# Kernel optimization log

Hardware: AMD Instinct MI355X
Metric: run time of the kernel (lower is better)

The kernel has to match this reference:

```python
import jax, jax.numpy as jnp
import numpy as np

B, N, IN_DIM = 32, 8192, 128
H, C = 4, 32
NEG_SLOPE = 0.2


def _xavier(key, shape, fan_in, fan_out):
    limit = np.sqrt(6.0 / (fan_in + fan_out))
    return jax.random.uniform(key, shape, minval=-limit, maxval=limit, dtype=jnp.float32)


def setup_inputs() -> dict:
    key = jax.random.key(0)
    k_x, k_wl, k_wr, k_att = jax.random.split(key, 4)
    x = jax.random.normal(k_x, (B, N, IN_DIM), dtype=jnp.float32)
    W_l = _xavier(k_wl, (IN_DIM, H * C), IN_DIM, H * C)
    b_l = jnp.zeros((H * C,), dtype=jnp.float32)
    W_r = _xavier(k_wr, (IN_DIM, H * C), IN_DIM, H * C)
    b_r = jnp.zeros((H * C,), dtype=jnp.float32)
    att = _xavier(k_att, (H, C), H, C)
    return {"x": x, "W_l": W_l, "b_l": b_l, "W_r": W_r, "b_r": b_r, "att": att}


def reference(x, W_l, b_l, W_r, b_r, att):
    Bs, Ns, _ = x.shape
    # Dense projections -> [B, N, H, C]
    x_l = (x @ W_l + b_l).reshape(Bs, Ns, H, C)
    x_r = (x @ W_r + b_r).reshape(Bs, Ns, H, C)
    # GATv2 additive score for edges (j -> center 0): LeakyReLU(x_l[0] + x_r[j])
    e = jax.nn.leaky_relu(x_l[:, :1, :, :] + x_r, negative_slope=NEG_SLOPE)  # [B,N,H,C]
    logits = jnp.einsum('bnhc,hc->bnh', e, att)  # [B,N,H]
    alpha = jax.nn.softmax(logits, axis=1)
    # Weighted aggregation into the center node; others keep their self-loop x_r
    m_center = jnp.sum(alpha[..., None] * x_r, axis=1, keepdims=True)  # [B,1,H,C]
    out = x_r.at[:, :1, :, :].set(m_center)
    return out.reshape(Bs, Ns, H * C)
```

## Files before the change

kernel.cpp:

```cpp
#include <hip/hip_runtime.h>

#define BATCH 32
#define NROWS 8192
#define IND   128
#define HC    128
#define NEG   0.2f
#define NBLK  32
#define ROWS  64
#define ITERS (NROWS / (NBLK * ROWS))
#define PART_STRIDE 136

typedef __attribute__((ext_vector_type(8))) short short8;
typedef __attribute__((ext_vector_type(4))) float f32x4;

#define BARRIER() asm volatile("s_waitcnt lgkmcnt(0)\n\ts_barrier" ::: "memory")

__device__ __forceinline__ unsigned short f2bf(float f) {
    unsigned u = __float_as_uint(f);
    u += 0x7FFFu + ((u >> 16) & 1u);
    return (unsigned short)(u >> 16);
}
__device__ __forceinline__ unsigned pack2(float a, float b) {
    return (unsigned)f2bf(a) | ((unsigned)f2bf(b) << 16);
}

__global__ void gat_center(const float* __restrict__ x, const float* __restrict__ Wl,
                           const float* __restrict__ bl, float* __restrict__ xl0)
{
    const int b = blockIdx.x, t = threadIdx.x;
    __shared__ float xrow[128];
    xrow[t] = x[(size_t)b * NROWS * IND + t];
    __syncthreads();
    float acc = bl[t];
#pragma unroll 16
    for (int k = 0; k < 128; ++k) acc = fmaf(xrow[k], Wl[k * 128 + t], acc);
    xl0[b * 128 + t] = acc;
}

__global__ __launch_bounds__(256, 3) void gat_main(
    const float* __restrict__ x, const float* __restrict__ Wr,
    const float* __restrict__ br, const float* __restrict__ att,
    const float* __restrict__ xl0, float* __restrict__ out,
    float* __restrict__ part)
{
    const int tid  = threadIdx.x;
    const int lane = tid & 63;
    const int wv   = tid >> 6;
    const int b    = blockIdx.x >> 5;
    const int blk  = blockIdx.x & (NBLK - 1);

    __shared__ float ubuf[64 * 132];
    __shared__ float w_s[64][4];
    __shared__ float wmax_s[4][4];
    __shared__ float wsum_s[4][4];
    __shared__ float Mrun_s[4], Srun_s[4], scale_s[4];
    __shared__ float Prun_s[128];
    __shared__ float ptmp_s[2][128];
    __shared__ float xl0_s[128], att_s[128], br_s[128];

    unsigned short* Asw = (unsigned short*)ubuf;
    float (*xr_s)[132]  = (float(*)[132])ubuf;

    const int pr[4] = { (tid) >> 4, (tid + 256) >> 4, (tid + 512) >> 4, (tid + 768) >> 4 };
    const int pk    = (tid & 15) << 3;

    float4 pf[4][2];
    {
        const float* xr0 = x + ((size_t)b * NROWS + blk * (ITERS * ROWS)) * IND;
#pragma unroll
        for (int ii = 0; ii < 4; ++ii) {
            pf[ii][0] = *(const float4*)(xr0 + pr[ii] * IND + pk);
            pf[ii][1] = *(const float4*)(xr0 + pr[ii] * IND + pk + 4);
        }
    }

    for (int i = tid; i < 128 * 128; i += 256) {
        int n = i & 127, k = i >> 7;
        Asw[n * 128 + (k ^ ((n & 7) << 3))] = f2bf(Wr[k * 128 + n]);
    }
    if (tid < 128) {
        xl0_s[tid]  = xl0[b * 128 + tid];
        att_s[tid]  = att[tid];
        br_s[tid]   = br[tid];
        Prun_s[tid] = 0.f;
    }
    if (tid < 4) { Mrun_s[tid] = -INFINITY; Srun_s[tid] = 0.f; }
    BARRIER();

    short8 bfr[2][4];
    {
        const int ksel = lane >> 4;
#pragma unroll
        for (int ct = 0; ct < 2; ++ct) {
            const int n  = wv * 32 + ct * 16 + (lane & 15);
            const int sw = (n & 7) << 3;
#pragma unroll
            for (int ks = 0; ks < 4; ++ks) {
                int k0 = ks * 32 + ksel * 8;
                bfr[ct][ks] = *(const short8*)&Asw[n * 128 + (k0 ^ sw)];
            }
        }
    }
    BARRIER();

    const int lr = tid >> 2, lh = tid & 3;

    for (int it = 0; it < ITERS; ++it) {
        const int n0 = blk * (ITERS * ROWS) + it * ROWS;

#pragma unroll
        for (int ii = 0; ii < 4; ++ii) {
            uint4 u;
            u.x = pack2(pf[ii][0].x, pf[ii][0].y); u.y = pack2(pf[ii][0].z, pf[ii][0].w);
            u.z = pack2(pf[ii][1].x, pf[ii][1].y); u.w = pack2(pf[ii][1].z, pf[ii][1].w);
            *(uint4*)&Asw[pr[ii] * 128 + (pk ^ ((pr[ii] & 7) << 3))] = u;
        }
        BARRIER();

        f32x4 acc[4][2];
#pragma unroll
        for (int i = 0; i < 4; ++i)
#pragma unroll
            for (int j = 0; j < 2; ++j) acc[i][j] = (f32x4){0.f, 0.f, 0.f, 0.f};
        {
            const int ksel = lane >> 4;
#pragma unroll
            for (int rt = 0; rt < 4; ++rt) {
                const int rA  = rt * 16 + (lane & 15);
                const int swa = (rA & 7) << 3;
                short8 afr[4];
#pragma unroll
                for (int ks = 0; ks < 4; ++ks) {
                    int k0 = ks * 32 + ksel * 8;
                    afr[ks] = *(const short8*)&Asw[rA * 128 + (k0 ^ swa)];
                }
#pragma unroll
                for (int ct = 0; ct < 2; ++ct)
#pragma unroll
                    for (int ks = 0; ks < 4; ++ks)
                        acc[rt][ct] = __builtin_amdgcn_mfma_f32_16x16x32_bf16(
                            afr[ks], bfr[ct][ks], acc[rt][ct], 0, 0, 0);
            }
        }
        BARRIER();

        {
            const int rq = (lane >> 4) * 4;
            const int cb = lane & 15;
#pragma unroll
            for (int rt = 0; rt < 4; ++rt)
#pragma unroll
                for (int ct = 0; ct < 2; ++ct) {
                    const int col  = wv * 32 + ct * 16 + cb;
                    const float bias = br_s[col];
#pragma unroll
                    for (int rg = 0; rg < 4; ++rg)
                        xr_s[rt * 16 + rq + rg][col] = acc[rt][ct][rg] + bias;
                }
        }
        BARRIER();

        if (it + 1 < ITERS) {
            const float* xr0 = x + ((size_t)b * NROWS + n0 + ROWS) * IND;
#pragma unroll
            for (int ii = 0; ii < 4; ++ii) {
                pf[ii][0] = *(const float4*)(xr0 + pr[ii] * IND + pk);
                pf[ii][1] = *(const float4*)(xr0 + pr[ii] * IND + pk + 4);
            }
        }

        {
            float* ob = out + ((size_t)b * NROWS + n0) * HC;
#pragma unroll
            for (int j = 0; j < 8; ++j) {
                int idx = tid + j * 256;
                int row = idx >> 5, c4 = (idx & 31) << 2;
                *(float4*)(ob + row * HC + c4) = *(const float4*)&xr_s[row][c4];
            }
        }

        float lg = 0.f;
        {
            const float* xp = &xr_s[lr][lh * 32];
            const float* ap = &att_s[lh * 32];
            const float* qp = &xl0_s[lh * 32];
#pragma unroll
            for (int c4 = 0; c4 < 32; c4 += 4) {
                float4 xv = *(const float4*)(xp + c4);
                float4 av = *(const float4*)(ap + c4);
                float4 qv = *(const float4*)(qp + c4);
                float v0 = qv.x + xv.x; v0 = v0 > 0.f ? v0 : NEG * v0;
                float v1 = qv.y + xv.y; v1 = v1 > 0.f ? v1 : NEG * v1;
                float v2 = qv.z + xv.z; v2 = v2 > 0.f ? v2 : NEG * v2;
                float v3 = qv.w + xv.w; v3 = v3 > 0.f ? v3 : NEG * v3;
                lg = fmaf(v0, av.x, fmaf(v1, av.y, fmaf(v2, av.z, fmaf(v3, av.w, lg))));
            }
        }

        float mx = lg;
#pragma unroll
        for (int mk = 4; mk < 64; mk <<= 1) mx = fmaxf(mx, __shfl_xor(mx, mk));
        if (lane < 4) wmax_s[wv][lane] = mx;
        BARRIER();

        const float Mblk = fmaxf(fmaxf(wmax_s[0][lh], wmax_s[1][lh]),
                                 fmaxf(wmax_s[2][lh], wmax_s[3][lh]));
        const float Mold = Mrun_s[lh];
        const float Mnew = fmaxf(Mold, Mblk);
        const float w    = __expf(lg - Mnew);
        w_s[lr][lh] = w;
        float swv = w;
#pragma unroll
        for (int mk = 4; mk < 64; mk <<= 1) swv += __shfl_xor(swv, mk);
        if (lane < 4) wsum_s[wv][lane] = swv;
        BARRIER();

        if (tid < 4) {
            const float sc = __expf(Mold - Mnew);
            scale_s[tid] = sc;
            Srun_s[tid]  = Srun_s[tid] * sc +
                (wsum_s[0][tid] + wsum_s[1][tid] + wsum_s[2][tid] + wsum_s[3][tid]);
            Mrun_s[tid]  = Mnew;
        }
        {
            const int hc = tid & 127, half = tid >> 7;
            const int h2 = hc >> 5;
            float accp = 0.f;
#pragma unroll 8
            for (int i2 = 0; i2 < 32; ++i2) {
                int rr = half * 32 + i2;
                accp = fmaf(w_s[rr][h2], xr_s[rr][hc], accp);
            }
            ptmp_s[half][hc] = accp;
        }
        BARRIER();
        if (tid < 128)
            Prun_s[tid] = Prun_s[tid] * scale_s[tid >> 5] + ptmp_s[0][tid] + ptmp_s[1][tid];
    }

    float* pb = part + (size_t)(b * NBLK + blk) * PART_STRIDE;
    if (tid < 4)   { pb[tid] = Mrun_s[tid]; pb[4 + tid] = Srun_s[tid]; }
    if (tid < 128) pb[8 + tid] = Prun_s[tid];
}

__global__ void gat_final(const float* __restrict__ part, float* __restrict__ out)
{
    const int b = blockIdx.x, t = threadIdx.x;
    const int h = t >> 5;
    const float* pb = part + (size_t)b * NBLK * PART_STRIDE;
    float Mg = -INFINITY;
    for (int i = 0; i < NBLK; ++i) Mg = fmaxf(Mg, pb[i * PART_STRIDE + h]);
    float Sg = 0.f, Pg = 0.f;
    for (int i = 0; i < NBLK; ++i) {
        const float sc = __expf(pb[i * PART_STRIDE + h] - Mg);
        Sg += pb[i * PART_STRIDE + 4 + h] * sc;
        Pg  = fmaf(pb[i * PART_STRIDE + 8 + t], sc, Pg);
    }
    out[(size_t)b * NROWS * HC + t] = Pg / Sg;
}

extern "C" void kernel_launch(void* const* d_in, const int* in_sizes, int n_in,
                              void* d_out, int out_size, void* d_ws, size_t ws_size,
                              hipStream_t stream)
{
    const float* x   = (const float*)d_in[0];
    const float* Wl  = (const float*)d_in[1];
    const float* bl  = (const float*)d_in[2];
    const float* Wr  = (const float*)d_in[3];
    const float* br  = (const float*)d_in[4];
    const float* att = (const float*)d_in[5];
    float* out = (float*)d_out;

    float* xl0  = (float*)d_ws;
    float* part = xl0 + BATCH * 128;

    gat_center<<<BATCH, 128, 0, stream>>>(x, Wl, bl, xl0);
    gat_main<<<BATCH * NBLK, 256, 0, stream>>>(x, Wr, br, att, xl0, out, part);
    gat_final<<<BATCH, 128, 0, stream>>>(part, out);
}
```

Measured before the change: 79.96 us.

## Split gat_main into more, smaller blocks and load W_r fragments directly from global

Raises the blocks per batch from 32 to 128, with 32-row tiles and 2 iterations, and raises the occupancy hint to 6 blocks per CU. Each block now builds its bf16 W_r MFMA fragments straight from global memory rather than transposing the whole matrix through LDS. Softmax running state moves from shared memory into registers, and several per-iteration barriers are removed. The aim is better latency hiding and cheaper per-block setup, at the cost of more partial records for the final reduction kernel to combine and redundant W_r reads across more blocks.

```diff
diff --git a/kernel.cpp b/kernel.cpp
--- a/kernel.cpp
+++ b/kernel.cpp
@@ -5,9 +5,9 @@
 #define IND   128
 #define HC    128
 #define NEG   0.2f
-#define NBLK  32
-#define ROWS  64
-#define ITERS (NROWS / (NBLK * ROWS))
+#define NBLK  128
+#define ROWS  32
+#define ITERS 2
 #define PART_STRIDE 136
 
 typedef __attribute__((ext_vector_type(8))) short short8;
@@ -37,7 +37,7 @@
     xl0[b * 128 + t] = acc;
 }
 
-__global__ __launch_bounds__(256, 3) void gat_main(
+__global__ __launch_bounds__(256, 6) void gat_main(
     const float* __restrict__ x, const float* __restrict__ Wr,
     const float* __restrict__ br, const float* __restrict__ att,
     const float* __restrict__ xl0, float* __restrict__ out,
@@ -46,86 +46,80 @@
     const int tid  = threadIdx.x;
     const int lane = tid & 63;
     const int wv   = tid >> 6;
-    const int b    = blockIdx.x >> 5;
+    const int b    = blockIdx.x >> 7;
     const int blk  = blockIdx.x & (NBLK - 1);
 
-    __shared__ float ubuf[64 * 132];
-    __shared__ float w_s[64][4];
-    __shared__ float wmax_s[4][4];
-    __shared__ float wsum_s[4][4];
-    __shared__ float Mrun_s[4], Srun_s[4], scale_s[4];
-    __shared__ float Prun_s[128];
+    __shared__ float ubuf[ROWS * 132];
+    __shared__ float wmax_s[2][4], wsum_s[2][4];
     __shared__ float ptmp_s[2][128];
-    __shared__ float xl0_s[128], att_s[128], br_s[128];
+    __shared__ float xl0_s[128], att_s[128];
 
     unsigned short* Asw = (unsigned short*)ubuf;
     float (*xr_s)[132]  = (float(*)[132])ubuf;
 
-    const int pr[4] = { (tid) >> 4, (tid + 256) >> 4, (tid + 512) >> 4, (tid + 768) >> 4 };
-    const int pk    = (tid & 15) << 3;
-
-    float4 pf[4][2];
+    const int pr0 = tid >> 4, pr1 = (tid + 256) >> 4;
+    const int pk  = (tid & 15) << 3;
+    const size_t xorg = ((size_t)b * NROWS + (size_t)blk * (ITERS * ROWS)) * IND;
+
+    float4 pf[2][2];
     {
-        const float* xr0 = x + ((size_t)b * NROWS + blk * (ITERS * ROWS)) * IND;
-#pragma unroll
-        for (int ii = 0; ii < 4; ++ii) {
-            pf[ii][0] = *(const float4*)(xr0 + pr[ii] * IND + pk);
-            pf[ii][1] = *(const float4*)(xr0 + pr[ii] * IND + pk + 4);
-        }
-    }
-
-    for (int i = tid; i < 128 * 128; i += 256) {
-        int n = i & 127, k = i >> 7;
-        Asw[n * 128 + (k ^ ((n & 7) << 3))] = f2bf(Wr[k * 128 + n]);
-    }
-    if (tid < 128) {
-        xl0_s[tid]  = xl0[b * 128 + tid];
-        att_s[tid]  = att[tid];
-        br_s[tid]   = br[tid];
-        Prun_s[tid] = 0.f;
-    }
-    if (tid < 4) { Mrun_s[tid] = -INFINITY; Srun_s[tid] = 0.f; }
-    BARRIER();
+        const float* s0 = x + xorg;
+        pf[0][0] = *(const float4*)(s0 + pr0 * IND + pk);
+        pf[0][1] = *(const float4*)(s0 + pr0 * IND + pk + 4);
+        pf[1][0] = *(const float4*)(s0 + pr1 * IND + pk);
+        pf[1][1] = *(const float4*)(s0 + pr1 * IND + pk + 4);
+    }
 
     short8 bfr[2][4];
     {
         const int ksel = lane >> 4;
 #pragma unroll
         for (int ct = 0; ct < 2; ++ct) {
-            const int n  = wv * 32 + ct * 16 + (lane & 15);
-            const int sw = (n & 7) << 3;
+            const int n = wv * 32 + ct * 16 + (lane & 15);
 #pragma unroll
             for (int ks = 0; ks < 4; ++ks) {
-                int k0 = ks * 32 + ksel * 8;
-                bfr[ct][ks] = *(const short8*)&Asw[n * 128 + (k0 ^ sw)];
-            }
-        }
-    }
-    BARRIER();
-
-    const int lr = tid >> 2, lh = tid & 3;
+                const int k0 = ks * 32 + ksel * 8;
+                const float* wp = Wr + (size_t)k0 * HC + n;
+                float v0 = wp[0 * HC], v1 = wp[1 * HC], v2 = wp[2 * HC], v3 = wp[3 * HC];
+                float v4 = wp[4 * HC], v5 = wp[5 * HC], v6 = wp[6 * HC], v7 = wp[7 * HC];
+                union { short8 s; unsigned u[4]; } t;
+                t.u[0] = pack2(v0, v1); t.u[1] = pack2(v2, v3);
+                t.u[2] = pack2(v4, v5); t.u[3] = pack2(v6, v7);
+                bfr[ct][ks] = t.s;
+            }
+        }
+    }
+    if (tid < 128) { xl0_s[tid] = xl0[b * 128 + tid]; att_s[tid] = att[tid]; }
+    const int   c0 = wv * 32 + (lane & 15), c1 = c0 + 16;
+    const float bi0 = br[c0], bi1 = br[c1];
+
+    const int lh = tid & 3;
+    const int hcp = tid & 127, half = tid >> 7;
+    const int hp  = hcp >> 5;
+
+    float Mrun = -INFINITY, Srun = 0.f, Prun = 0.f;
 
     for (int it = 0; it < ITERS; ++it) {
-        const int n0 = blk * (ITERS * ROWS) + it * ROWS;
-
-#pragma unroll
-        for (int ii = 0; ii < 4; ++ii) {
-            uint4 u;
-            u.x = pack2(pf[ii][0].x, pf[ii][0].y); u.y = pack2(pf[ii][0].z, pf[ii][0].w);
-            u.z = pack2(pf[ii][1].x, pf[ii][1].y); u.w = pack2(pf[ii][1].z, pf[ii][1].w);
-            *(uint4*)&Asw[pr[ii] * 128 + (pk ^ ((pr[ii] & 7) << 3))] = u;
-        }
-        BARRIER();
-
-        f32x4 acc[4][2];
-#pragma unroll
-        for (int i = 0; i < 4; ++i)
+        {
+            uint4 u0, u1;
+            u0.x = pack2(pf[0][0].x, pf[0][0].y); u0.y = pack2(pf[0][0].z, pf[0][0].w);
+            u0.z = pack2(pf[0][1].x, pf[0][1].y); u0.w = pack2(pf[0][1].z, pf[0][1].w);
+            u1.x = pack2(pf[1][0].x, pf[1][0].y); u1.y = pack2(pf[1][0].z, pf[1][0].w);
+            u1.z = pack2(pf[1][1].x, pf[1][1].y); u1.w = pack2(pf[1][1].z, pf[1][1].w);
+            *(uint4*)&Asw[pr0 * 128 + (pk ^ ((pr0 & 7) << 3))] = u0;
+            *(uint4*)&Asw[pr1 * 128 + (pk ^ ((pr1 & 7) << 3))] = u1;
+        }
+        BARRIER();
+
+        f32x4 acc[2][2];
+#pragma unroll
+        for (int i = 0; i < 2; ++i)
 #pragma unroll
             for (int j = 0; j < 2; ++j) acc[i][j] = (f32x4){0.f, 0.f, 0.f, 0.f};
         {
             const int ksel = lane >> 4;
 #pragma unroll
-            for (int rt = 0; rt < 4; ++rt) {
+            for (int rt = 0; rt < 2; ++rt) {
                 const int rA  = rt * 16 + (lane & 15);
                 const int swa = (rA & 7) << 3;
                 short8 afr[4];
@@ -146,41 +140,37 @@
 
         {
             const int rq = (lane >> 4) * 4;
-            const int cb = lane & 15;
-#pragma unroll
-            for (int rt = 0; rt < 4; ++rt)
-#pragma unroll
-                for (int ct = 0; ct < 2; ++ct) {
-                    const int col  = wv * 32 + ct * 16 + cb;
-                    const float bias = br_s[col];
-#pragma unroll
-                    for (int rg = 0; rg < 4; ++rg)
-                        xr_s[rt * 16 + rq + rg][col] = acc[rt][ct][rg] + bias;
+#pragma unroll
+            for (int rt = 0; rt < 2; ++rt)
+#pragma unroll
+                for (int rg = 0; rg < 4; ++rg) {
+                    xr_s[rt * 16 + rq + rg][c0] = acc[rt][0][rg] + bi0;
+                    xr_s[rt * 16 + rq + rg][c1] = acc[rt][1][rg] + bi1;
                 }
         }
         BARRIER();
 
         if (it + 1 < ITERS) {
-            const float* xr0 = x + ((size_t)b * NROWS + n0 + ROWS) * IND;
-#pragma unroll
-            for (int ii = 0; ii < 4; ++ii) {
-                pf[ii][0] = *(const float4*)(xr0 + pr[ii] * IND + pk);
-                pf[ii][1] = *(const float4*)(xr0 + pr[ii] * IND + pk + 4);
-            }
-        }
-
-        {
-            float* ob = out + ((size_t)b * NROWS + n0) * HC;
-#pragma unroll
-            for (int j = 0; j < 8; ++j) {
+            const float* s1 = x + xorg + (size_t)(it + 1) * ROWS * IND;
+            pf[0][0] = *(const float4*)(s1 + pr0 * IND + pk);
+            pf[0][1] = *(const float4*)(s1 + pr0 * IND + pk + 4);
+            pf[1][0] = *(const float4*)(s1 + pr1 * IND + pk);
+            pf[1][1] = *(const float4*)(s1 + pr1 * IND + pk + 4);
+        }
+
+        {
+            float* ob = out + ((size_t)b * NROWS + (size_t)blk * (ITERS * ROWS) + it * ROWS) * HC;
+#pragma unroll
+            for (int j = 0; j < 4; ++j) {
                 int idx = tid + j * 256;
-                int row = idx >> 5, c4 = (idx & 31) << 2;
-                *(float4*)(ob + row * HC + c4) = *(const float4*)&xr_s[row][c4];
-            }
-        }
-
-        float lg = 0.f;
-        {
+                int row = idx >> 5, cc = (idx & 31) << 2;
+                *(float4*)(ob + row * HC + cc) = *(const float4*)&xr_s[row][cc];
+            }
+        }
+
+        float lg = 0.f, w = 0.f;
+        if (tid < 128) {
+            const int lr = tid >> 2;
             const float* xp = &xr_s[lr][lh * 32];
             const float* ap = &att_s[lh * 32];
             const float* qp = &xl0_s[lh * 32];
@@ -195,52 +185,49 @@
                 float v3 = qv.w + xv.w; v3 = v3 > 0.f ? v3 : NEG * v3;
                 lg = fmaf(v0, av.x, fmaf(v1, av.y, fmaf(v2, av.z, fmaf(v3, av.w, lg))));
             }
-        }
-
-        float mx = lg;
-#pragma unroll
-        for (int mk = 4; mk < 64; mk <<= 1) mx = fmaxf(mx, __shfl_xor(mx, mk));
-        if (lane < 4) wmax_s[wv][lane] = mx;
-        BARRIER();
-
-        const float Mblk = fmaxf(fmaxf(wmax_s[0][lh], wmax_s[1][lh]),
-                                 fmaxf(wmax_s[2][lh], wmax_s[3][lh]));
-        const float Mold = Mrun_s[lh];
-        const float Mnew = fmaxf(Mold, Mblk);
-        const float w    = __expf(lg - Mnew);
-        w_s[lr][lh] = w;
-        float swv = w;
-#pragma unroll
-        for (int mk = 4; mk < 64; mk <<= 1) swv += __shfl_xor(swv, mk);
-        if (lane < 4) wsum_s[wv][lane] = swv;
-        BARRIER();
-
-        if (tid < 4) {
-            const float sc = __expf(Mold - Mnew);
-            scale_s[tid] = sc;
-            Srun_s[tid]  = Srun_s[tid] * sc +
-                (wsum_s[0][tid] + wsum_s[1][tid] + wsum_s[2][tid] + wsum_s[3][tid]);
-            Mrun_s[tid]  = Mnew;
-        }
-        {
-            const int hc = tid & 127, half = tid >> 7;
-            const int h2 = hc >> 5;
+            float mx = lg;
+#pragma unroll
+            for (int mk = 4; mk < 64; mk <<= 1) mx = fmaxf(mx, __shfl_xor(mx, mk));
+            if (lane < 4) wmax_s[wv][lane] = mx;
+        }
+        BARRIER();
+
+        if (tid < 128) {
+            const float Mb   = fmaxf(wmax_s[0][lh], wmax_s[1][lh]);
+            const float Mnew = fmaxf(Mrun, Mb);
+            w = __expf(lg - Mnew);
+            float swv = w;
+#pragma unroll
+            for (int mk = 4; mk < 64; mk <<= 1) swv += __shfl_xor(swv, mk);
+            if (lane < 4) wsum_s[wv][lane] = swv;
+            ptmp_s[0][tid] = w;
+        }
+        BARRIER();
+
+        {
+            const float Mb   = fmaxf(wmax_s[0][hp], wmax_s[1][hp]);
+            const float Mnew = fmaxf(Mrun, Mb);
+            const float sc   = __expf(Mrun - Mnew);
+            Srun = Srun * sc + (wsum_s[0][hp] + wsum_s[1][hp]);
             float accp = 0.f;
-#pragma unroll 8
-            for (int i2 = 0; i2 < 32; ++i2) {
-                int rr = half * 32 + i2;
-                accp = fmaf(w_s[rr][h2], xr_s[rr][hc], accp);
-            }
-            ptmp_s[half][hc] = accp;
-        }
-        BARRIER();
-        if (tid < 128)
-            Prun_s[tid] = Prun_s[tid] * scale_s[tid >> 5] + ptmp_s[0][tid] + ptmp_s[1][tid];
-    }
-
+#pragma unroll
+            for (int i2 = 0; i2 < 16; ++i2) {
+                const int rr = half * 16 + i2;
+                accp = fmaf(ptmp_s[0][rr * 4 + hp], xr_s[rr][hcp], accp);
+            }
+            Prun = Prun * sc + accp;
+            Mrun = Mnew;
+        }
+        BARRIER();
+    }
+
+    ptmp_s[half][hcp] = Prun;
+    BARRIER();
     float* pb = part + (size_t)(b * NBLK + blk) * PART_STRIDE;
-    if (tid < 4)   { pb[tid] = Mrun_s[tid]; pb[4 + tid] = Srun_s[tid]; }
-    if (tid < 128) pb[8 + tid] = Prun_s[tid];
+    if (tid < 128) {
+        if ((hcp & 31) == 0) { pb[hp] = Mrun; pb[4 + hp] = Srun; }
+        pb[8 + hcp] = ptmp_s[0][hcp] + ptmp_s[1][hcp];
+    }
 }
 
 __global__ void gat_final(const float* __restrict__ part, float* __restrict__ out)
@@ -249,8 +236,10 @@
     const int h = t >> 5;
     const float* pb = part + (size_t)b * NBLK * PART_STRIDE;
     float Mg = -INFINITY;
+#pragma unroll 4
     for (int i = 0; i < NBLK; ++i) Mg = fmaxf(Mg, pb[i * PART_STRIDE + h]);
     float Sg = 0.f, Pg = 0.f;
+#pragma unroll 4
     for (int i = 0; i < NBLK; ++i) {
         const float sc = __expf(pb[i * PART_STRIDE + h] - Mg);
         Sg += pb[i * PART_STRIDE + 4 + h] * sc;
```

Result: slower. 224.2 us (+180.5%).
